# Kernel tuning notes

Measured on AMD Instinct MI355X. Metric: run time of the kernel, lower is better.

The kernel has to match this reference:

```python
import jax, jax.numpy as jnp
import numpy as np

BH, S, D = 32, 2048, 128

def setup_inputs() -> dict:
    key = jax.random.key(0)
    k1, k2, k3, k4 = jax.random.split(key, 4)
    q = jax.random.normal(k1, (BH, S, D), dtype=jnp.float32)
    k = jax.random.normal(k2, (BH, S, D), dtype=jnp.float32)
    v = jax.random.normal(k3, (BH, S, D), dtype=jnp.float32)
    scale_factor = jax.random.normal(k4, (S, S), dtype=jnp.float32)
    return {"q": q, "k": k, "v": v, "scale_factor": scale_factor, "dropout_p": 1}

def reference(q, k, v, scale_factor, dropout_p):
    # qk: [BH, Sq, Sk]
    qk = jnp.einsum('bqd,bkd->bqk', q, k)
    scaled_qk = qk * scale_factor  # per-element (non-scalar) scale, broadcast over BH
    p = jax.nn.softmax(scaled_qk, axis=-1)
    # Dropout(p=0.0) is identity; then mul by scalar dropout_p
    p = p * dropout_p
    out = jnp.einsum('bqk,bkd->bqd', p, v)
    return out
```

## Files before the change

### kernel.cpp

```cpp
#include <hip/hip_runtime.h>

#define S_LEN 2048
#define D_DIM 128
#define BQ 128
#define BK 32
#define NITER (S_LEN / BK)

typedef float f32x4 __attribute__((ext_vector_type(4)));
typedef short s16x8 __attribute__((ext_vector_type(8)));
typedef short s16x4 __attribute__((ext_vector_type(4)));
typedef unsigned int u32;

#if __has_builtin(__builtin_amdgcn_exp2f)
#define EXP2(x) __builtin_amdgcn_exp2f(x)
#else
#define EXP2(x) exp2f(x)
#endif

__device__ __forceinline__ u32 pack_trunc(float x0, float x1) {
    return __builtin_amdgcn_perm(__float_as_uint(x1), __float_as_uint(x0), 0x07060302u);
}
__device__ __forceinline__ u32 pack_rne(float x0, float x1) {
    return __builtin_amdgcn_perm(__float_as_uint(x1) + 0x8000u,
                                 __float_as_uint(x0) + 0x8000u, 0x07060302u);
}

#define GLOAD16(g, l) \
    __builtin_amdgcn_global_load_lds((const __attribute__((address_space(1))) u32*)(g), \
                                     (__attribute__((address_space(3))) u32*)(l), 16, 0, 0)

#if __has_builtin(__builtin_amdgcn_mfma_f32_16x16x16bf16_1k)
__device__ __forceinline__ f32x4 MFMA16(s16x4 a, s16x4 b, f32x4 c) {
    return __builtin_amdgcn_mfma_f32_16x16x16bf16_1k(a, b, c, 0, 0, 0);
}
#else
__device__ __forceinline__ f32x4 MFMA16(s16x4 a, s16x4 b, f32x4 c) {
    asm("v_mfma_f32_16x16x16_bf16 %0, %1, %2, %0" : "+v"(c) : "v"(a), "v"(b));
    return c;
}
#endif

__global__ void prep_k(const float* __restrict__ K, unsigned short* __restrict__ Kc) {
    const int t  = blockIdx.x * 256 + threadIdx.x;
    const int c  = t & 15;
    const int s  = (t >> 4) & (S_LEN - 1);
    const int bh = t >> 15;
    const float* src = K + ((size_t)bh * S_LEN + s) * D_DIM + c * 8;
    const float4 a = *(const float4*)src;
    const float4 b = *(const float4*)(src + 4);
    const float x[8] = {a.x,a.y,a.z,a.w,b.x,b.y,b.z,b.w};
    u32 h[4], l[4];
    #pragma unroll
    for (int i = 0; i < 4; ++i) {
        const float x0 = x[2*i], x1 = x[2*i+1];
        h[i] = pack_trunc(x0, x1);
        const float r0 = x0 - __uint_as_float(__float_as_uint(x0) & 0xFFFF0000u);
        const float r1 = x1 - __uint_as_float(__float_as_uint(x1) & 0xFFFF0000u);
        l[i] = pack_trunc(r0, r1);
    }
    const int kt = s >> 5, r = s & 31, rl = r & 7;
    unsigned short* base = Kc + ((((size_t)bh * NITER + kt) * 32 + r) << 8);
    *(uint4*)(base + (((2*c)     ^ rl) << 3)) = make_uint4(h[0],h[1],h[2],h[3]);
    *(uint4*)(base + (((2*c + 1) ^ rl) << 3)) = make_uint4(l[0],l[1],l[2],l[3]);
}

__global__ void prep_v(const float* __restrict__ V, unsigned short* __restrict__ Vt) {
    const int t  = blockIdx.x * 256 + threadIdx.x;
    const int d  = t & 127;
    const int kt = (t >> 7) & (NITER - 1);
    const int bh = t >> 13;
    const float* src = V + (((size_t)bh * NITER + kt) * BK) * D_DIM + d;
    u32 wv[16];
    #pragma unroll
    for (int i = 0; i < 16; ++i)
        wv[i] = pack_rne(src[(2*i) * D_DIM], src[(2*i+1) * D_DIM]);
    unsigned short* dst = Vt + ((((size_t)bh * NITER + kt) * D_DIM + d) << 5);
    const int vs = (d >> 1) & 3;
    #pragma unroll
    for (int i = 0; i < 4; ++i)
        *(uint4*)(dst + ((i ^ vs) << 3)) = make_uint4(wv[4*i],wv[4*i+1],wv[4*i+2],wv[4*i+3]);
}

__global__ __launch_bounds__(256, 2)
void attn_fused(const float* __restrict__ Q, const unsigned short* __restrict__ Kc,
                const unsigned short* __restrict__ Vt, const float* __restrict__ SF,
                const int* __restrict__ DP, float* __restrict__ OUT)
{
    __shared__ __align__(16) unsigned short sK[2][32 * 256];
    __shared__ __align__(16) unsigned short sVt[2][128 * 32];

    const int bh   = blockIdx.y;
    const int q0   = blockIdx.x * BQ;
    const int tid  = threadIdx.x;
    const int w    = tid >> 6;
    const int lane = tid & 63;
    const int quad = lane >> 4;
    const int lr   = lane & 15;
    const int rl   = lr & 7;

    const size_t bh_off = (size_t)bh * S_LEN * D_DIM;
    const float LOG2E = 1.4426950408889634f;

    s16x8 qhi[2][4], qlo[2][4];
    int qrow[2];
    #pragma unroll
    for (int g = 0; g < 2; ++g) {
        qrow[g] = q0 + w * 32 + g * 16 + lr;
        const float* qr = Q + bh_off + (size_t)qrow[g] * D_DIM + quad * 8;
        #pragma unroll
        for (int d0 = 0; d0 < 4; ++d0) {
            const float4 u0 = *(const float4*)(qr + d0 * 32);
            const float4 u1 = *(const float4*)(qr + d0 * 32 + 4);
            const float x[8] = {u0.x,u0.y,u0.z,u0.w,u1.x,u1.y,u1.z,u1.w};
            union { u32 w4[4]; s16x8 v; } H, L;
            #pragma unroll
            for (int i = 0; i < 4; ++i) {
                const float x0 = x[2*i], x1 = x[2*i+1];
                H.w4[i] = pack_trunc(x0, x1);
                const float r0 = x0 - __uint_as_float(__float_as_uint(x0) & 0xFFFF0000u);
                const float r1 = x1 - __uint_as_float(__float_as_uint(x1) & 0xFFFF0000u);
                L.w4[i] = pack_trunc(r0, r1);
            }
            qhi[g][d0] = H.v; qlo[g][d0] = L.v;
        }
    }

    f32x4 Oacc[2][8] = {};
    float mrow[2] = {-INFINITY, -INFINITY};
    float lrow[2] = {0.f, 0.f};

    const unsigned short* KtBase = Kc + (((size_t)bh * NITER) << 13);
    const unsigned short* VtBase = Vt + (((size_t)bh * NITER) << 12);

    const int vsl  = (lr >> 1) & 3;
    const int off0 = ((((quad >> 1))     ^ vsl) << 4) + (quad & 1) * 8;
    const int off1 = (((2 + (quad >> 1)) ^ vsl) << 4) + (quad & 1) * 8;

    #pragma unroll
    for (int i = 0; i < 4; ++i)
        GLOAD16(KtBase + (w * 4 + i) * 512 + lane * 8, &sK[0][(w * 4 + i) * 512]);
    #pragma unroll
    for (int i = 0; i < 2; ++i)
        GLOAD16(VtBase + (w * 2 + i) * 512 + lane * 8, &sVt[0][(w * 2 + i) * 512]);

    const float* sfq[2];
    f32x4 sf0[2], sf1[2];
    {
        const f32x4 l2e = {LOG2E, LOG2E, LOG2E, LOG2E};
        #pragma unroll
        for (int g = 0; g < 2; ++g) {
            sfq[g] = SF + (size_t)qrow[g] * S_LEN + quad * 4;
            sf0[g] = *(const f32x4*)(sfq[g]) * l2e;
            sf1[g] = *(const f32x4*)(sfq[g] + 16) * l2e;
        }
    }

    for (int kt = 0; kt < NITER; ++kt) {
        const int p = kt & 1;
        __syncthreads();

        f32x4 nf0[2], nf1[2];
        const bool more = (kt + 1 < NITER);
        if (more) {
            const unsigned short* Kn = KtBase + ((size_t)(kt + 1) << 13);
            const unsigned short* Vn = VtBase + ((size_t)(kt + 1) << 12);
            #pragma unroll
            for (int i = 0; i < 4; ++i)
                GLOAD16(Kn + (w * 4 + i) * 512 + lane * 8, &sK[1 - p][(w * 4 + i) * 512]);
            #pragma unroll
            for (int i = 0; i < 2; ++i)
                GLOAD16(Vn + (w * 2 + i) * 512 + lane * 8, &sVt[1 - p][(w * 2 + i) * 512]);
            const f32x4 l2e = {LOG2E, LOG2E, LOG2E, LOG2E};
            #pragma unroll
            for (int g = 0; g < 2; ++g) {
                nf0[g] = *(const f32x4*)(sfq[g] + (kt + 1) * 32) * l2e;
                nf1[g] = *(const f32x4*)(sfq[g] + (kt + 1) * 32 + 16) * l2e;
            }
        }

        const unsigned short* sKp = sK[p];
        f32x4 acc[2][2] = {};
        __builtin_amdgcn_s_setprio(1);
        #pragma unroll
        for (int nt = 0; nt < 2; ++nt) {
            const unsigned short* rowp = sKp + (nt * 16 + lr) * 256;
            #pragma unroll
            for (int d0 = 0; d0 < 4; ++d0) {
                const int uh = (8 * d0 + 2 * quad) ^ rl;
                const s16x8 kh8 = *(const s16x8*)(rowp + (uh << 3));
                const s16x8 kl8 = *(const s16x8*)(rowp + ((uh ^ 1) << 3));
                #pragma unroll
                for (int g = 0; g < 2; ++g) {
                    acc[g][nt] = __builtin_amdgcn_mfma_f32_16x16x32_bf16(kh8, qlo[g][d0], acc[g][nt], 0, 0, 0);
                    acc[g][nt] = __builtin_amdgcn_mfma_f32_16x16x32_bf16(kl8, qhi[g][d0], acc[g][nt], 0, 0, 0);
                    acc[g][nt] = __builtin_amdgcn_mfma_f32_16x16x32_bf16(kh8, qhi[g][d0], acc[g][nt], 0, 0, 0);
                }
            }
        }
        __builtin_amdgcn_s_setprio(0);

        union PB { u32 w2[2]; s16x4 v; } B0[2], B1[2];
        #pragma unroll
        for (int g = 0; g < 2; ++g) {
            const f32x4 t0 = acc[g][0] * sf0[g];
            const f32x4 t1 = acc[g][1] * sf1[g];
            float mx = fmaxf(fmaxf(fmaxf(t0[0], t0[1]), fmaxf(t0[2], t0[3])),
                             fmaxf(fmaxf(t1[0], t1[1]), fmaxf(t1[2], t1[3])));
            mx = fmaxf(mx, __shfl_xor(mx, 16));
            mx = fmaxf(mx, __shfl_xor(mx, 32));
            const float mnew = fmaxf(mrow[g], mx);
            if (!__all(mnew == mrow[g])) {
                const float al = EXP2(mrow[g] - mnew);
                mrow[g] = mnew;
                lrow[g] *= al;
                const f32x4 alv = {al, al, al, al};
                #pragma unroll
                for (int dt = 0; dt < 8; ++dt)
                    Oacc[g][dt] *= alv;
            }
            const float m = mrow[g];
            f32x4 P0, P1;
            #pragma unroll
            for (int r = 0; r < 4; ++r) {
                P0[r] = EXP2(t0[r] - m);
                P1[r] = EXP2(t1[r] - m);
            }
            float rs = ((P0[0] + P0[1]) + (P0[2] + P0[3])) + ((P1[0] + P1[1]) + (P1[2] + P1[3]));
            rs += __shfl_xor(rs, 16);
            rs += __shfl_xor(rs, 32);
            lrow[g] += rs;
            B0[g].w2[0] = pack_rne(P0[0], P0[1]); B0[g].w2[1] = pack_rne(P0[2], P0[3]);
            B1[g].w2[0] = pack_rne(P1[0], P1[1]); B1[g].w2[1] = pack_rne(P1[2], P1[3]);
        }

        const unsigned short* sVp = sVt[p];
        __builtin_amdgcn_s_setprio(1);
        #pragma unroll
        for (int dt = 0; dt < 8; ++dt) {
            const char* vrow = (const char*)(sVp + (dt * 16 + lr) * 32);
            const s16x4 va0 = *(const s16x4*)(vrow + off0);
            const s16x4 va1 = *(const s16x4*)(vrow + off1);
            #pragma unroll
            for (int g = 0; g < 2; ++g) {
                Oacc[g][dt] = MFMA16(va0, B0[g].v, Oacc[g][dt]);
                Oacc[g][dt] = MFMA16(va1, B1[g].v, Oacc[g][dt]);
            }
        }
        __builtin_amdgcn_s_setprio(0);

        if (more) {
            #pragma unroll
            for (int g = 0; g < 2; ++g) { sf0[g] = nf0[g]; sf1[g] = nf1[g]; }
        }
    }

    const float dpf = (float)DP[0];
    #pragma unroll
    for (int g = 0; g < 2; ++g) {
        const float sc = dpf / lrow[g];
        const f32x4 scv = {sc, sc, sc, sc};
        float* orow = OUT + bh_off + (size_t)qrow[g] * D_DIM + quad * 4;
        #pragma unroll
        for (int dt = 0; dt < 8; ++dt) {
            const f32x4 o = Oacc[g][dt] * scv;
            *(f32x4*)(orow + dt * 16) = o;
        }
    }
}

extern "C" void kernel_launch(void* const* d_in, const int* in_sizes, int n_in,
                              void* d_out, int out_size, void* d_ws, size_t ws_size,
                              hipStream_t stream) {
    const float* q  = (const float*)d_in[0];
    const float* k  = (const float*)d_in[1];
    const float* v  = (const float*)d_in[2];
    const float* sf = (const float*)d_in[3];
    const int*   dp = (const int*)d_in[4];
    float* out = (float*)d_out;

    const size_t kc_ushorts = (size_t)32 * NITER * 32 * 256;
    unsigned short* Kc = (unsigned short*)d_ws;
    unsigned short* Vt = Kc + kc_ushorts;

    prep_k<<<4096, 256, 0, stream>>>(k, Kc);
    prep_v<<<1024, 256, 0, stream>>>(v, Vt);
    dim3 grid(S_LEN / BQ, 32);
    attn_fused<<<grid, dim3(256), 0, stream>>>(q, Kc, Vt, sf, dp, out);
}
```

Before: 315.6 us.

## Load V fragments directly from global into registers, drop V shared memory staging

Reorganizes the V preprocessing layout so each lane's MFMA operand fragment for a 16-wide d tile is one contiguous 16-byte chunk. The attention kernel then loads V per iteration straight from global memory into registers, removing the LDS double buffer and its reads. It also swaps the cross-lane max/sum reductions to permlane swap builtins when they are available. The change cuts LDS usage and traffic but exposes global load latency within each iteration, since V is no longer prefetched one tile ahead.

```diff
diff --git a/kernel.cpp b/kernel.cpp
--- a/kernel.cpp
+++ b/kernel.cpp
@@ -39,6 +39,23 @@
     return c;
 }
 #endif
+
+#if __has_builtin(__builtin_amdgcn_permlane16_swap) && __has_builtin(__builtin_amdgcn_permlane32_swap)
+#define BFLY(x, OP)                                                                       \
+    {                                                                                     \
+        auto p_ = __builtin_amdgcn_permlane16_swap(__float_as_uint(x), __float_as_uint(x), false, false); \
+        x = OP(__uint_as_float(p_[0]), __uint_as_float(p_[1]));                           \
+        auto q_ = __builtin_amdgcn_permlane32_swap(__float_as_uint(x), __float_as_uint(x), false, false); \
+        x = OP(__uint_as_float(q_[0]), __uint_as_float(q_[1]));                           \
+    }
+#else
+#define BFLY(x, OP)                      \
+    {                                    \
+        x = OP(x, __shfl_xor(x, 16));    \
+        x = OP(x, __shfl_xor(x, 32));    \
+    }
+#endif
+__device__ __forceinline__ float fadd_(float a, float b) { return a + b; }
 
 __global__ void prep_k(const float* __restrict__ K, unsigned short* __restrict__ Kc) {
     const int t  = blockIdx.x * 256 + threadIdx.x;
@@ -70,15 +87,16 @@
     const int kt = (t >> 7) & (NITER - 1);
     const int bh = t >> 13;
     const float* src = V + (((size_t)bh * NITER + kt) * BK) * D_DIM + d;
-    u32 wv[16];
-    #pragma unroll
-    for (int i = 0; i < 16; ++i)
-        wv[i] = pack_rne(src[(2*i) * D_DIM], src[(2*i+1) * D_DIM]);
-    unsigned short* dst = Vt + ((((size_t)bh * NITER + kt) * D_DIM + d) << 5);
-    const int vs = (d >> 1) & 3;
-    #pragma unroll
-    for (int i = 0; i < 4; ++i)
-        *(uint4*)(dst + ((i ^ vs) << 3)) = make_uint4(wv[4*i],wv[4*i+1],wv[4*i+2],wv[4*i+3]);
+    const int dt = d >> 4, lr = d & 15;
+    unsigned short* base = Vt + ((((size_t)bh * NITER + kt) * 8 + dt) << 9);
+    #pragma unroll
+    for (int q = 0; q < 4; ++q) {
+        u32 w0 = pack_rne(src[(q*4+0) * D_DIM],    src[(q*4+1) * D_DIM]);
+        u32 w1 = pack_rne(src[(q*4+2) * D_DIM],    src[(q*4+3) * D_DIM]);
+        u32 w2 = pack_rne(src[(16+q*4+0) * D_DIM], src[(16+q*4+1) * D_DIM]);
+        u32 w3 = pack_rne(src[(16+q*4+2) * D_DIM], src[(16+q*4+3) * D_DIM]);
+        *(uint4*)(base + ((q * 16 + lr) << 3)) = make_uint4(w0, w1, w2, w3);
+    }
 }
 
 __global__ __launch_bounds__(256, 2)
@@ -87,7 +105,6 @@
                 const int* __restrict__ DP, float* __restrict__ OUT)
 {
     __shared__ __align__(16) unsigned short sK[2][32 * 256];
-    __shared__ __align__(16) unsigned short sVt[2][128 * 32];
 
     const int bh   = blockIdx.y;
     const int q0   = blockIdx.x * BQ;
@@ -130,18 +147,11 @@
     float lrow[2] = {0.f, 0.f};
 
     const unsigned short* KtBase = Kc + (((size_t)bh * NITER) << 13);
-    const unsigned short* VtBase = Vt + (((size_t)bh * NITER) << 12);
-
-    const int vsl  = (lr >> 1) & 3;
-    const int off0 = ((((quad >> 1))     ^ vsl) << 4) + (quad & 1) * 8;
-    const int off1 = (((2 + (quad >> 1)) ^ vsl) << 4) + (quad & 1) * 8;
+    const unsigned short* VtBase = Vt + (((size_t)bh * NITER) << 12) + (lane << 3);
 
     #pragma unroll
     for (int i = 0; i < 4; ++i)
         GLOAD16(KtBase + (w * 4 + i) * 512 + lane * 8, &sK[0][(w * 4 + i) * 512]);
-    #pragma unroll
-    for (int i = 0; i < 2; ++i)
-        GLOAD16(VtBase + (w * 2 + i) * 512 + lane * 8, &sVt[0][(w * 2 + i) * 512]);
 
     const float* sfq[2];
     f32x4 sf0[2], sf1[2];
@@ -159,17 +169,21 @@
         const int p = kt & 1;
         __syncthreads();
 
+        uint4 vreg[8];
+        {
+            const unsigned short* Vk = VtBase + ((size_t)kt << 12);
+            #pragma unroll
+            for (int dt = 0; dt < 8; ++dt)
+                vreg[dt] = *(const uint4*)(Vk + (dt << 9));
+        }
+
         f32x4 nf0[2], nf1[2];
         const bool more = (kt + 1 < NITER);
         if (more) {
             const unsigned short* Kn = KtBase + ((size_t)(kt + 1) << 13);
-            const unsigned short* Vn = VtBase + ((size_t)(kt + 1) << 12);
             #pragma unroll
             for (int i = 0; i < 4; ++i)
                 GLOAD16(Kn + (w * 4 + i) * 512 + lane * 8, &sK[1 - p][(w * 4 + i) * 512]);
-            #pragma unroll
-            for (int i = 0; i < 2; ++i)
-                GLOAD16(Vn + (w * 2 + i) * 512 + lane * 8, &sVt[1 - p][(w * 2 + i) * 512]);
             const f32x4 l2e = {LOG2E, LOG2E, LOG2E, LOG2E};
             #pragma unroll
             for (int g = 0; g < 2; ++g) {
@@ -206,8 +220,7 @@
             const f32x4 t1 = acc[g][1] * sf1[g];
             float mx = fmaxf(fmaxf(fmaxf(t0[0], t0[1]), fmaxf(t0[2], t0[3])),
                              fmaxf(fmaxf(t1[0], t1[1]), fmaxf(t1[2], t1[3])));
-            mx = fmaxf(mx, __shfl_xor(mx, 16));
-            mx = fmaxf(mx, __shfl_xor(mx, 32));
+            BFLY(mx, fmaxf);
             const float mnew = fmaxf(mrow[g], mx);
             if (!__all(mnew == mrow[g])) {
                 const float al = EXP2(mrow[g] - mnew);
@@ -226,24 +239,21 @@
                 P1[r] = EXP2(t1[r] - m);
             }
             float rs = ((P0[0] + P0[1]) + (P0[2] + P0[3])) + ((P1[0] + P1[1]) + (P1[2] + P1[3]));
-            rs += __shfl_xor(rs, 16);
-            rs += __shfl_xor(rs, 32);
+            BFLY(rs, fadd_);
             lrow[g] += rs;
             B0[g].w2[0] = pack_rne(P0[0], P0[1]); B0[g].w2[1] = pack_rne(P0[2], P0[3]);
             B1[g].w2[0] = pack_rne(P1[0], P1[1]); B1[g].w2[1] = pack_rne(P1[2], P1[3]);
         }
 
-        const unsigned short* sVp = sVt[p];
         __builtin_amdgcn_s_setprio(1);
         #pragma unroll
         for (int dt = 0; dt < 8; ++dt) {
-            const char* vrow = (const char*)(sVp + (dt * 16 + lr) * 32);
-            const s16x4 va0 = *(const s16x4*)(vrow + off0);
-            const s16x4 va1 = *(const s16x4*)(vrow + off1);
+            union { uint4 u; struct { s16x4 a0; s16x4 a1; } s; } vv;
+            vv.u = vreg[dt];
             #pragma unroll
             for (int g = 0; g < 2; ++g) {
-                Oacc[g][dt] = MFMA16(va0, B0[g].v, Oacc[g][dt]);
-                Oacc[g][dt] = MFMA16(va1, B1[g].v, Oacc[g][dt]);
+                Oacc[g][dt] = MFMA16(vv.s.a0, B0[g].v, Oacc[g][dt]);
+                Oacc[g][dt] = MFMA16(vv.s.a1, B1[g].v, Oacc[g][dt]);
             }
         }
         __builtin_amdgcn_s_setprio(0);
```

Result: no change. 312.3 us (-1.1%).
